# Optimization experiments

Measured on AMD Instinct MI355X. Metric: run time of the kernel, lower is better.

## Reference

```python
import math
import jax, jax.numpy as jnp
import numpy as np

EMB = 512        # emb_size
MAXW = 1024      # max_width
MAXH = 1024      # max_height
P_DROP = 0.1     # dropout prob
NUM_BOXES = 1024
BATCH = 64


def setup_inputs() -> dict:
    key = jax.random.key(0)
    k1, k2 = jax.random.split(key)
    src_embedding = jax.random.normal(k1, (NUM_BOXES, BATCH, EMB), dtype=jnp.float32)
    # box coords in [0, max_width] / [0, max_height] inclusive
    src_boxes = jax.random.randint(k2, (BATCH, NUM_BOXES, 4), 0, MAXW + 1, dtype=jnp.int32)
    return {"src_embedding": src_embedding, "src_boxes": src_boxes}


def _sin_tables():
    d4 = EMB // 4
    # den = exp(-arange(emb/4) * log(10000) / emb / 4)  (matches torch precedence)
    den = jnp.exp(-jnp.arange(d4, dtype=jnp.float32) * math.log(10000.0) / EMB / 4)
    x_pe = jnp.sin(jnp.arange(MAXW + 1, dtype=jnp.float32)[:, None] * den)  # (MAXW+1, d4)
    y_pe = jnp.sin(jnp.arange(MAXH + 1, dtype=jnp.float32)[:, None] * den)  # (MAXH+1, d4)
    return x_pe, y_pe


def _get_pe(src_boxes):
    # src_boxes: (B, N, 4) int. Returns pe: (N, B, EMB)
    x_pe, y_pe = _sin_tables()
    g0 = x_pe[src_boxes[..., 0]]  # (B, N, d4) -> lanes 0::4
    g1 = y_pe[src_boxes[..., 1]]  # lanes 1::4
    g2 = x_pe[src_boxes[..., 2]]  # lanes 2::4
    g3 = y_pe[src_boxes[..., 3]]  # lanes 3::4
    B, N = src_boxes.shape[0], src_boxes.shape[1]
    # stacking on last axis then flattening interleaves exactly like 0::4,1::4,2::4,3::4
    pe = jnp.stack([g0, g1, g2, g3], axis=-1).reshape(B, N, EMB)
    return jnp.transpose(pe, (1, 0, 2))  # (N, B, EMB)


def reference(src_embedding, src_boxes):
    x = src_embedding + _get_pe(src_boxes)
    # training-mode dropout with fixed key (deterministic reference)
    keep = jax.random.bernoulli(jax.random.key(42), 1.0 - P_DROP, x.shape)
    return jnp.where(keep, x / (1.0 - P_DROP), jnp.zeros((), x.dtype))
```

## Files before the change

### kernel.cpp

```cpp
#include <hip/hip_runtime.h>


namespace {

constexpr int      NBOX     = 1024;
constexpr unsigned TOTAL_G  = 1024u * 64u * 128u;
constexpr unsigned NBLK     = 2048;
constexpr unsigned NTHR     = 256;
constexpr unsigned STRIDE_G = NBLK * NTHR;
constexpr int      ITERS    = TOTAL_G / STRIDE_G;

__device__ __forceinline__ unsigned rotl(unsigned x, int r) {
  return __builtin_amdgcn_alignbit(x, x, 32 - r);
}

__device__ __forceinline__ unsigned threefry_xor(unsigned ctr) {
  unsigned x0 = 0u;
  unsigned x1 = ctr + 42u;
#define R4(a,b,c,d)                       \
  x0 += x1; x1 = rotl(x1,(a)) ^ x0;       \
  x0 += x1; x1 = rotl(x1,(b)) ^ x0;       \
  x0 += x1; x1 = rotl(x1,(c)) ^ x0;       \
  x0 += x1; x1 = rotl(x1,(d)) ^ x0;
  R4(13,15,26,6)
  x0 += 42u;          x1 += 0x1BD11BF1u;
  R4(17,29,16,24)
  x0 += 0x1BD11BF0u;  x1 += 2u;
  R4(13,15,26,6)
         x1 += 45u;
  R4(17,29,16,24)
  x0 += 42u;          x1 += 0x1BD11BF4u;
  R4(13,15,26,6)
  x0 += 0x1BD11BF0u;  x1 += 5u;
#undef R4
  return x0 ^ x1;
}

__global__ __launch_bounds__(256) void pe_add_dropout(
    const float4* __restrict__ emb,
    const int4*   __restrict__ boxes,
    float4*       __restrict__ out) {
  const float K2 = 0.0064881408103268795f;
  const float SC = 1.11111111111111111f;

  unsigned g = blockIdx.x * NTHR + threadIdx.x;
  const unsigned j    = g & 127u;
  const unsigned row0 = g >> 7;
  const unsigned b    = row0 & 63u;
  const unsigned n0   = row0 >> 6;

  const float den = exp2f(-(float)j * K2);
  const int4* bp  = boxes + (b * NBOX + n0);
  unsigned i0 = g << 2;

#pragma unroll 2
  for (int it = 0; it < ITERS; ++it) {
    const float4 e  = emb[g];
    const int4   bx = *bp;

    const float s0 = __sinf((float)bx.x * den);
    const float s1 = __sinf((float)bx.y * den);
    const float s2 = __sinf((float)bx.z * den);
    const float s3 = __sinf((float)bx.w * den);

    const unsigned m0 = threefry_xor(i0);
    const unsigned m1 = threefry_xor(i0 + 1u);
    const unsigned m2 = threefry_xor(i0 + 2u);
    const unsigned m3 = threefry_xor(i0 + 3u);

    float4 r;
    r.x = (m0 < 3865470464u) ? (e.x + s0) * SC : 0.0f;
    r.y = (m1 < 3865470464u) ? (e.y + s1) * SC : 0.0f;
    r.z = (m2 < 3865470464u) ? (e.z + s2) * SC : 0.0f;
    r.w = (m3 < 3865470464u) ? (e.w + s3) * SC : 0.0f;
    out[g] = r;

    g  += STRIDE_G;
    bp += 64;
    i0 += STRIDE_G * 4u;
  }
}

}

extern "C" void kernel_launch(void* const* d_in, const int* in_sizes, int n_in,
                              void* d_out, int out_size, void* d_ws, size_t ws_size,
                              hipStream_t stream) {
  const float4* emb   = (const float4*)d_in[0];
  const int4*   boxes = (const int4*)d_in[1];
  float4*       outp  = (float4*)d_out;
  hipLaunchKernelGGL(pe_add_dropout, dim3(NBLK), dim3(NTHR), 0, stream,
                     emb, boxes, outp);
}
```

Baseline: 78.53 us.

## Prefetch next embedding, scalarize box loads, nontemporal stores, more blocks

```diff
diff --git a/kernel.cpp b/kernel.cpp
--- a/kernel.cpp
+++ b/kernel.cpp
@@ -3,9 +3,11 @@
 
 namespace {
 
+typedef float f32x4 __attribute__((ext_vector_type(4)));
+
 constexpr int      NBOX     = 1024;
 constexpr unsigned TOTAL_G  = 1024u * 64u * 128u;
-constexpr unsigned NBLK     = 2048;
+constexpr unsigned NBLK     = 8192;
 constexpr unsigned NTHR     = 256;
 constexpr unsigned STRIDE_G = NBLK * NTHR;
 constexpr int      ITERS    = TOTAL_G / STRIDE_G;
@@ -37,46 +39,48 @@
 }
 
 __global__ __launch_bounds__(256) void pe_add_dropout(
-    const float4* __restrict__ emb,
-    const int4*   __restrict__ boxes,
-    float4*       __restrict__ out) {
+    const f32x4* __restrict__ emb,
+    const int*   __restrict__ boxes,
+    f32x4*       __restrict__ out) {
   const float K2 = 0.0064881408103268795f;
   const float SC = 1.11111111111111111f;
 
   unsigned g = blockIdx.x * NTHR + threadIdx.x;
-  const unsigned j    = g & 127u;
-  const unsigned row0 = g >> 7;
-  const unsigned b    = row0 & 63u;
-  const unsigned n0   = row0 >> 6;
+  const unsigned j = g & 127u;
+  const float den = exp2f(-(float)j * K2);
+  unsigned i0 = g << 2;
 
-  const float den = exp2f(-(float)j * K2);
-  const int4* bp  = boxes + (b * NBOX + n0);
-  unsigned i0 = g << 2;
+  f32x4 e = emb[g];
 
 #pragma unroll 2
   for (int it = 0; it < ITERS; ++it) {
-    const float4 e  = emb[g];
-    const int4   bx = *bp;
+    const unsigned g_next = g + STRIDE_G;
+    const unsigned g_pf   = g_next < TOTAL_G ? g_next : (TOTAL_G - 1u);
+    const f32x4 e_next = emb[g_pf];
 
-    const float s0 = __sinf((float)bx.x * den);
-    const float s1 = __sinf((float)bx.y * den);
-    const float s2 = __sinf((float)bx.z * den);
-    const float s3 = __sinf((float)bx.w * den);
+    const unsigned row = __builtin_amdgcn_readfirstlane(g >> 7);
+    const int* bq = boxes + (((row & 63u) * NBOX + (row >> 6)) << 2);
+    const int b0 = bq[0], b1 = bq[1], b2 = bq[2], b3 = bq[3];
+
+    const float s0 = __sinf((float)b0 * den);
+    const float s1 = __sinf((float)b1 * den);
+    const float s2 = __sinf((float)b2 * den);
+    const float s3 = __sinf((float)b3 * den);
 
     const unsigned m0 = threefry_xor(i0);
     const unsigned m1 = threefry_xor(i0 + 1u);
     const unsigned m2 = threefry_xor(i0 + 2u);
     const unsigned m3 = threefry_xor(i0 + 3u);
 
-    float4 r;
+    f32x4 r;
     r.x = (m0 < 3865470464u) ? (e.x + s0) * SC : 0.0f;
     r.y = (m1 < 3865470464u) ? (e.y + s1) * SC : 0.0f;
     r.z = (m2 < 3865470464u) ? (e.z + s2) * SC : 0.0f;
     r.w = (m3 < 3865470464u) ? (e.w + s3) * SC : 0.0f;
-    out[g] = r;
+    __builtin_nontemporal_store(r, &out[g]);
 
-    g  += STRIDE_G;
-    bp += 64;
+    e  = e_next;
+    g  = g_next;
     i0 += STRIDE_G * 4u;
   }
 }
@@ -86,9 +90,9 @@
 extern "C" void kernel_launch(void* const* d_in, const int* in_sizes, int n_in,
                               void* d_out, int out_size, void* d_ws, size_t ws_size,
                               hipStream_t stream) {
-  const float4* emb   = (const float4*)d_in[0];
-  const int4*   boxes = (const int4*)d_in[1];
-  float4*       outp  = (float4*)d_out;
+  const f32x4* emb   = (const f32x4*)d_in[0];
+  const int*   boxes = (const int*)d_in[1];
+  f32x4*       outp  = (f32x4*)d_out;
   hipLaunchKernelGGL(pe_add_dropout, dim3(NBLK), dim3(NTHR), 0, stream,
                      emb, boxes, outp);
 }
```

New measurement: 84.91 us. 1.08x slower.
